# Kernel optimization log

Hardware: AMD Instinct MI355X
Metric: run time of the kernel (lower is better)

The kernel has to match this reference:

```python
import jax, jax.numpy as jnp
import numpy as np

N = 50000      # nodes
E = 800000     # edges (before self loops)
F_IN = 128     # num_features
D = 128        # d_graph_layer
L = 3          # n_graph_layer (extra GAT layers after conv1)
DFC = 128      # d_FC_layer
NFC = 2        # n_FC_layer
C = 2          # num_classes
G = 1000       # number of graphs
NEG_SLOPE = 0.2


def setup_inputs() -> dict:
    key = jax.random.key(0)
    ks = jax.random.split(key, 24)
    s = lambda d: 1.0 / np.sqrt(d)
    inp = {
        "x": jax.random.normal(ks[0], (N, F_IN), jnp.float32),
        "energy": jax.random.normal(ks[1], (G, 1), jnp.float32),
        # conv1 params
        "W1": jax.random.normal(ks[2], (F_IN, D), jnp.float32) * s(F_IN),
        "as1": jax.random.normal(ks[3], (D,), jnp.float32) * s(D),
        "ad1": jax.random.normal(ks[4], (D,), jnp.float32) * s(D),
        "b1": jnp.zeros((D,), jnp.float32),
        # stacked convs params
        "Ws": jax.random.normal(ks[5], (L, D, D), jnp.float32) * s(D),
        "ass": jax.random.normal(ks[6], (L, D), jnp.float32) * s(D),
        "ads": jax.random.normal(ks[7], (L, D), jnp.float32) * s(D),
        "bs": jnp.zeros((L, D), jnp.float32),
        # FC head
        "lin0_W": jax.random.normal(ks[8], (D, DFC), jnp.float32) * s(D),
        "lin0_b": jnp.zeros((DFC,), jnp.float32),
        "lin1_W": jax.random.normal(ks[9], (DFC + 1, DFC), jnp.float32) * s(DFC + 1),
        "lin1_b": jnp.zeros((DFC,), jnp.float32),
        "lins_W": jax.random.normal(ks[10], (NFC - 1, DFC, DFC), jnp.float32) * s(DFC),
        "lins_b": jnp.zeros((NFC - 1, DFC), jnp.float32),
        "lin3_W": jax.random.normal(ks[11], (DFC, C), jnp.float32) * s(DFC),
        "lin3_b": jnp.zeros((C,), jnp.float32),
        # graph structure
        "edge_index": jax.random.randint(ks[12], (2, E), 0, N, dtype=jnp.int64),
        "batchs": jnp.sort(jax.random.randint(ks[13], (N,), 0, G, dtype=jnp.int64)),
    }
    return inp


def gat_layer(x, W, a_src, a_dst, b, src, dst):
    # GATConv (heads=1): h = xW; e_ij = LeakyReLU(a_src.h_src + a_dst.h_dst);
    # alpha = softmax over edges grouped by dst; out_i = sum alpha * h_src + b
    h = x @ W                                        # [N, D]
    e = jax.nn.leaky_relu((h @ a_src)[src] + (h @ a_dst)[dst], NEG_SLOPE)  # [E']
    m = jax.ops.segment_max(e, dst, num_segments=N)  # every node has a self loop
    w = jnp.exp(e - m[dst])
    denom = jax.ops.segment_sum(w, dst, num_segments=N)
    alpha = w / denom[dst]
    out = jax.ops.segment_sum(h[src] * alpha[:, None], dst, num_segments=N)
    return out + b


def reference(x, energy, W1, as1, ad1, b1, Ws, ass, ads, bs,
              lin0_W, lin0_b, lin1_W, lin1_b, lins_W, lins_b,
              lin3_W, lin3_b, edge_index, batchs):
    loop = jnp.arange(N, dtype=edge_index.dtype)     # GATConv add_self_loops
    src = jnp.concatenate([edge_index[0], loop])
    dst = jnp.concatenate([edge_index[1], loop])

    h = jax.nn.relu(gat_layer(x, W1, as1, ad1, b1, src, dst))
    for i in range(L):
        h = jax.nn.relu(gat_layer(h, Ws[i], ass[i], ads[i], bs[i], src, dst))

    g = jax.ops.segment_sum(h, batchs, num_segments=G)   # global_add_pool [G, D]
    y = jax.nn.relu(g @ lin0_W + lin0_b)                 # lins[0]
    z = jax.nn.relu(jnp.concatenate([y, energy], axis=1) @ lin1_W + lin1_b)
    z = z + y                                            # residual
    for i in range(NFC - 1):
        z = jax.nn.relu(z @ lins_W[i] + lins_b[i])
    logits = z @ lin3_W + lin3_b
    return jax.nn.log_softmax(logits, axis=1)            # last == 'log'
```

## Files before the change

kernel.cpp:

```cpp
#include <hip/hip_runtime.h>
#include <math.h>

#define NN 50000
#define EE 800000
#define ET 850000
#define DD 128
#define GG 1000
#define SLOPE 0.2f

typedef unsigned int  u32;
typedef unsigned short u16;

__device__ __forceinline__ u16 f2h(float f){
  return __builtin_bit_cast(unsigned short, (_Float16)f);
}
__device__ __forceinline__ float hlo(u32 d){
  return (float)__builtin_bit_cast(_Float16, (unsigned short)(d & 0xFFFFu));
}
__device__ __forceinline__ float hhi(u32 d){
  return (float)__builtin_bit_cast(_Float16, (unsigned short)(d >> 16));
}

__global__ void init_k(const int* __restrict__ batchs, int* __restrict__ cnt,
                       int* __restrict__ gstart){
  int n = blockIdx.x*256 + threadIdx.x;
  if (n < NN){
    cnt[n] = 0;
    int b = batchs[n];
    int prev = n ? batchs[n-1] : -1;
    for (int g = prev+1; g <= b; ++g) gstart[g] = n;
    if (n == NN-1){
      for (int g = b+1; g <= GG; ++g) gstart[g] = NN;
    }
  }
}

__global__ void count_k(const int* __restrict__ ei, int* __restrict__ cnt){
  int e = blockIdx.x*256 + threadIdx.x;
  if (e < ET){
    int d = (e < EE) ? ei[EE + e] : (e - EE);
    atomicAdd(&cnt[d], 1);
  }
}

__global__ __launch_bounds__(256) void blocksum_k(const int* __restrict__ cnt,
                                                  int* __restrict__ bsum){
  int i = blockIdx.x*256 + threadIdx.x;
  int v = (i < NN) ? cnt[i] : 0;
  #pragma unroll
  for (int o=32;o;o>>=1) v += __shfl_xor(v,o);
  __shared__ int ws[4];
  if ((threadIdx.x & 63) == 0) ws[threadIdx.x>>6] = v;
  __syncthreads();
  if (threadIdx.x == 0) bsum[blockIdx.x] = ws[0]+ws[1]+ws[2]+ws[3];
}

__global__ __launch_bounds__(256) void scanb_k(int* __restrict__ bsum, int nb){
  int tid = threadIdx.x;
  int v = (tid < nb) ? bsum[tid] : 0;
  int lane = tid & 63, wv = tid >> 6;
  int s = v;
  #pragma unroll
  for (int o=1;o<64;o<<=1){ int t = __shfl_up(s,o); if (lane>=o) s += t; }
  __shared__ int ws[4];
  if (lane == 63) ws[wv] = s;
  __syncthreads();
  int woff = 0;
  for (int k=0;k<wv;++k) woff += ws[k];
  if (tid < nb) bsum[tid] = s - v + woff;
}

__global__ __launch_bounds__(256) void scatter_k(const int* __restrict__ cnt,
                                                 const int* __restrict__ bsum,
                                                 int* __restrict__ row_start,
                                                 int* __restrict__ cursor){
  int i = blockIdx.x*256 + threadIdx.x;
  int v = (i < NN) ? cnt[i] : 0;
  int lane = threadIdx.x & 63, wv = threadIdx.x >> 6;
  int s = v;
  #pragma unroll
  for (int o=1;o<64;o<<=1){ int t = __shfl_up(s,o); if (lane>=o) s += t; }
  __shared__ int ws[4];
  if (lane == 63) ws[wv] = s;
  __syncthreads();
  int woff = 0;
  for (int k=0;k<wv;++k) woff += ws[k];
  int off = s - v + woff + bsum[blockIdx.x];
  if (i < NN){ row_start[i] = off; cursor[i] = off; }
  if (i == 0) row_start[NN] = ET;
}

__global__ void fill_k(const int* __restrict__ ei, int* __restrict__ cursor,
                       int* __restrict__ srcs){
  int e = blockIdx.x*256 + threadIdx.x;
  if (e < ET){
    int s, d;
    if (e < EE){ s = ei[e]; d = ei[EE + e]; }
    else       { s = e - EE; d = s; }
    int pos = atomicAdd(&cursor[d], 1);
    srcs[pos] = s;
  }
}

__global__ __launch_bounds__(256) void gemm128_f_k(const float* __restrict__ A,
                                                   const float* __restrict__ W,
                                                   const float* __restrict__ as,
                                                   const float* __restrict__ ad,
                                                   float* __restrict__ C,
                                                   float* __restrict__ hs,
                                                   float* __restrict__ hd){
  __shared__ float Alt[DD*64];
  __shared__ float Wl[DD*64];
  int tid = threadIdx.x;
  int rbase = blockIdx.x*64;
  for (int it=0; it<8; ++it){
    int i = it*256 + tid;
    int r = i & 63;
    int c4 = i >> 6;
    float4 v = {0.f,0.f,0.f,0.f};
    if (rbase + r < NN) v = *(const float4*)(A + (size_t)(rbase+r)*DD + c4*4);
    Alt[(c4*4+0)*64 + r] = v.x;
    Alt[(c4*4+1)*64 + r] = v.y;
    Alt[(c4*4+2)*64 + r] = v.z;
    Alt[(c4*4+3)*64 + r] = v.w;
  }
  int ry = tid >> 4, cx = tid & 15;
  float hsum[4] = {0.f,0.f,0.f,0.f};
  float hdsum[4] = {0.f,0.f,0.f,0.f};
  for (int jt=0; jt<2; ++jt){
    __syncthreads();
    for (int it=0; it<8; ++it){
      int i = it*256 + tid;
      int k = i >> 4, c4 = i & 15;
      *(float4*)(Wl + k*64 + c4*4) = *(const float4*)(W + k*DD + jt*64 + c4*4);
    }
    __syncthreads();
    float acc[4][4] = {};
    #pragma unroll 8
    for (int k=0;k<DD;++k){
      float4 av = *(const float4*)(Alt + k*64 + ry*4);
      float4 wv = *(const float4*)(Wl + k*64 + cx*4);
      float a[4] = {av.x, av.y, av.z, av.w};
      float b[4] = {wv.x, wv.y, wv.z, wv.w};
      #pragma unroll
      for (int ii=0;ii<4;++ii)
        #pragma unroll
        for (int jj=0;jj<4;++jj)
          acc[ii][jj] += a[ii]*b[jj];
    }
    float4 a_s = *(const float4*)(as + jt*64 + cx*4);
    float4 a_d = *(const float4*)(ad + jt*64 + cx*4);
    #pragma unroll
    for (int ii=0;ii<4;++ii){
      float ds = acc[ii][0]*a_s.x + acc[ii][1]*a_s.y + acc[ii][2]*a_s.z + acc[ii][3]*a_s.w;
      float dd = acc[ii][0]*a_d.x + acc[ii][1]*a_d.y + acc[ii][2]*a_d.z + acc[ii][3]*a_d.w;
      #pragma unroll
      for (int o=1;o<16;o<<=1){ ds += __shfl_xor(ds,o); dd += __shfl_xor(dd,o); }
      hsum[ii] += ds; hdsum[ii] += dd;
    }
    #pragma unroll
    for (int ii=0;ii<4;++ii){
      int r = rbase + ry*4 + ii;
      if (r < NN){
        float4 o = {acc[ii][0], acc[ii][1], acc[ii][2], acc[ii][3]};
        *(float4*)(C + (size_t)r*DD + jt*64 + cx*4) = o;
      }
    }
  }
  if (cx == 0){
    #pragma unroll
    for (int ii=0;ii<4;++ii){
      int r = rbase + ry*4 + ii;
      if (r < NN){ hs[r] = hsum[ii]; hd[r] = hdsum[ii]; }
    }
  }
}

__global__ __launch_bounds__(256) void gemm128_h_k(const float* __restrict__ A,
                                                   const float* __restrict__ W,
                                                   const float* __restrict__ as,
                                                   const float* __restrict__ ad,
                                                   u16* __restrict__ Ch,
                                                   float* __restrict__ hs,
                                                   float* __restrict__ hd){
  __shared__ float Alt[DD*64];
  __shared__ float Wl[DD*64];
  int tid = threadIdx.x;
  int rbase = blockIdx.x*64;
  for (int it=0; it<8; ++it){
    int i = it*256 + tid;
    int r = i & 63;
    int c4 = i >> 6;
    float4 v = {0.f,0.f,0.f,0.f};
    if (rbase + r < NN) v = *(const float4*)(A + (size_t)(rbase+r)*DD + c4*4);
    Alt[(c4*4+0)*64 + r] = v.x;
    Alt[(c4*4+1)*64 + r] = v.y;
    Alt[(c4*4+2)*64 + r] = v.z;
    Alt[(c4*4+3)*64 + r] = v.w;
  }
  int ry = tid >> 4, cx = tid & 15;
  float hsum[4] = {0.f,0.f,0.f,0.f};
  float hdsum[4] = {0.f,0.f,0.f,0.f};
  for (int jt=0; jt<2; ++jt){
    __syncthreads();
    for (int it=0; it<8; ++it){
      int i = it*256 + tid;
      int k = i >> 4, c4 = i & 15;
      *(float4*)(Wl + k*64 + c4*4) = *(const float4*)(W + k*DD + jt*64 + c4*4);
    }
    __syncthreads();
    float acc[4][4] = {};
    #pragma unroll 8
    for (int k=0;k<DD;++k){
      float4 av = *(const float4*)(Alt + k*64 + ry*4);
      float4 wv = *(const float4*)(Wl + k*64 + cx*4);
      float a[4] = {av.x, av.y, av.z, av.w};
      float b[4] = {wv.x, wv.y, wv.z, wv.w};
      #pragma unroll
      for (int ii=0;ii<4;++ii)
        #pragma unroll
        for (int jj=0;jj<4;++jj)
          acc[ii][jj] += a[ii]*b[jj];
    }
    float4 a_s = *(const float4*)(as + jt*64 + cx*4);
    float4 a_d = *(const float4*)(ad + jt*64 + cx*4);
    #pragma unroll
    for (int ii=0;ii<4;++ii){
      float ds = acc[ii][0]*a_s.x + acc[ii][1]*a_s.y + acc[ii][2]*a_s.z + acc[ii][3]*a_s.w;
      float dd = acc[ii][0]*a_d.x + acc[ii][1]*a_d.y + acc[ii][2]*a_d.z + acc[ii][3]*a_d.w;
      #pragma unroll
      for (int o=1;o<16;o<<=1){ ds += __shfl_xor(ds,o); dd += __shfl_xor(dd,o); }
      hsum[ii] += ds; hdsum[ii] += dd;
    }
    #pragma unroll
    for (int ii=0;ii<4;++ii){
      int r = rbase + ry*4 + ii;
      if (r < NN){
        ushort4 o;
        o.x = f2h(acc[ii][0]); o.y = f2h(acc[ii][1]);
        o.z = f2h(acc[ii][2]); o.w = f2h(acc[ii][3]);
        *(ushort4*)(Ch + (size_t)r*DD + jt*64 + cx*4) = o;
      }
    }
  }
  if (cx == 0){
    #pragma unroll
    for (int ii=0;ii<4;++ii){
      int r = rbase + ry*4 + ii;
      if (r < NN){ hs[r] = hsum[ii]; hd[r] = hdsum[ii]; }
    }
  }
}

__global__ __launch_bounds__(256) void gat_agg_f_k(const float* __restrict__ h,
                                                   const float* __restrict__ hs,
                                                   const float* __restrict__ hd,
                                                   const int* __restrict__ row_start,
                                                   const int* __restrict__ srcs,
                                                   const float* __restrict__ bias,
                                                   float* __restrict__ out){
  int node = blockIdx.x*4 + (threadIdx.x >> 6);
  int lane = threadIdx.x & 63;
  if (node >= NN) return;
  int half = lane >> 5;
  int hl   = lane & 31;
  int beg = row_start[node], end = row_start[node+1];
  float hdn = hd[node];
  float m = -INFINITY, denom = 0.f;
  float4 acc = {0.f,0.f,0.f,0.f};
  for (int c=beg; c<end; c+=64){
    int nc = min(64, end-c);
    float e = -INFINITY; int src = 0;
    if (lane < nc){
      src = srcs[c+lane];
      float t = hs[src] + hdn;
      e = (t >= 0.f) ? t : SLOPE*t;
    }
    float cm = e;
    #pragma unroll
    for (int o=32;o;o>>=1) cm = fmaxf(cm, __shfl_xor(cm,o));
    float nm = fmaxf(m, cm);
    float w = (lane < nc) ? expf(e - nm) : 0.f;
    float cs = w;
    #pragma unroll
    for (int o=32;o;o>>=1) cs += __shfl_xor(cs,o);
    float scale = expf(m - nm);
    denom = denom*scale + cs;
    acc.x *= scale; acc.y *= scale; acc.z *= scale; acc.w *= scale;
    m = nm;
    int nh = (nc + 1 - half) >> 1;
    for (int i=0;i<nh;++i){
      int j = 2*i + half;
      float wi = __shfl(w, j);
      int   si = __shfl(src, j);
      float4 hv = *(const float4*)(h + (size_t)si*DD + hl*4);
      acc.x += wi*hv.x; acc.y += wi*hv.y; acc.z += wi*hv.z; acc.w += wi*hv.w;
    }
  }
  acc.x += __shfl_xor(acc.x, 32);
  acc.y += __shfl_xor(acc.y, 32);
  acc.z += __shfl_xor(acc.z, 32);
  acc.w += __shfl_xor(acc.w, 32);
  if (half == 0){
    float inv = 1.f/denom;
    float4 b4 = *(const float4*)(bias + hl*4);
    float4 o4;
    o4.x = fmaxf(acc.x*inv + b4.x, 0.f);
    o4.y = fmaxf(acc.y*inv + b4.y, 0.f);
    o4.z = fmaxf(acc.z*inv + b4.z, 0.f);
    o4.w = fmaxf(acc.w*inv + b4.w, 0.f);
    *(float4*)(out + (size_t)node*DD + hl*4) = o4;
  }
}

__global__ __launch_bounds__(256) void gat_agg_h_k(const u16* __restrict__ hh,
                                                   const float* __restrict__ hs,
                                                   const float* __restrict__ hd,
                                                   const int* __restrict__ row_start,
                                                   const int* __restrict__ srcs,
                                                   const float* __restrict__ bias,
                                                   float* __restrict__ out){
  int node = blockIdx.x*4 + (threadIdx.x >> 6);
  int lane = threadIdx.x & 63;
  if (node >= NN) return;
  int half = lane >> 5;
  int hl   = lane & 31;
  int beg = row_start[node], end = row_start[node+1];
  float hdn = hd[node];
  float m = -INFINITY, denom = 0.f;
  float a0=0.f, a1=0.f, a2=0.f, a3=0.f;
  for (int c=beg; c<end; c+=64){
    int nc = min(64, end-c);
    float e = -INFINITY; int src = 0;
    if (lane < nc){
      src = srcs[c+lane];
      float t = hs[src] + hdn;
      e = (t >= 0.f) ? t : SLOPE*t;
    }
    float cm = e;
    #pragma unroll
    for (int o=32;o;o>>=1) cm = fmaxf(cm, __shfl_xor(cm,o));
    float nm = fmaxf(m, cm);
    float w = (lane < nc) ? expf(e - nm) : 0.f;
    float cs = w;
    #pragma unroll
    for (int o=32;o;o>>=1) cs += __shfl_xor(cs,o);
    float scale = expf(m - nm);
    denom = denom*scale + cs;
    a0 *= scale; a1 *= scale; a2 *= scale; a3 *= scale;
    m = nm;
    int nh = (nc + 1 - half) >> 1;
    for (int i=0;i<nh;++i){
      int j = 2*i + half;
      float wi = __shfl(w, j);
      int   si = __shfl(src, j);
      uint2 hv = *(const uint2*)(hh + (size_t)si*DD + hl*4);
      a0 += wi*hlo(hv.x); a1 += wi*hhi(hv.x);
      a2 += wi*hlo(hv.y); a3 += wi*hhi(hv.y);
    }
  }
  a0 += __shfl_xor(a0, 32);
  a1 += __shfl_xor(a1, 32);
  a2 += __shfl_xor(a2, 32);
  a3 += __shfl_xor(a3, 32);
  if (half == 0){
    float inv = 1.f/denom;
    float4 b4 = *(const float4*)(bias + hl*4);
    float4 o4;
    o4.x = fmaxf(a0*inv + b4.x, 0.f);
    o4.y = fmaxf(a1*inv + b4.y, 0.f);
    o4.z = fmaxf(a2*inv + b4.z, 0.f);
    o4.w = fmaxf(a3*inv + b4.w, 0.f);
    *(float4*)(out + (size_t)node*DD + hl*4) = o4;
  }
}

__global__ __launch_bounds__(128) void tail_k(const float* __restrict__ h,
                                              const int* __restrict__ gstart,
                                              const float* __restrict__ energy,
                                              const float* __restrict__ W0, const float* __restrict__ b0,
                                              const float* __restrict__ W1, const float* __restrict__ b1,
                                              const float* __restrict__ W2, const float* __restrict__ b2,
                                              const float* __restrict__ W3, const float* __restrict__ b3,
                                              float* __restrict__ out){
  __shared__ float row[DD];
  __shared__ float buf[DD];
  int gr = blockIdx.x, j = threadIdx.x;
  int beg = gstart[gr], end = gstart[gr+1];
  float s = 0.f;
  for (int n=beg; n<end; ++n) s += h[(size_t)n*DD + j];
  row[j] = s;
  __syncthreads();
  float acc = 0.f;
  #pragma unroll 8
  for (int k=0;k<DD;++k) acc += row[k]*W0[k*DD + j];
  float y = fmaxf(acc + b0[j], 0.f);
  buf[j] = y;
  __syncthreads();
  acc = 0.f;
  #pragma unroll 8
  for (int k=0;k<DD;++k) acc += buf[k]*W1[k*DD + j];
  acc += energy[gr]*W1[DD*DD + j];
  float z = fmaxf(acc + b1[j], 0.f) + y;
  __syncthreads();
  row[j] = z;
  __syncthreads();
  acc = 0.f;
  #pragma unroll 8
  for (int k=0;k<DD;++k) acc += row[k]*W2[k*DD + j];
  float z2 = fmaxf(acc + b2[j], 0.f);
  buf[j] = z2;
  __syncthreads();
  if (j < 64){
    float z0 = buf[j], z1 = buf[j+64];
    float l0 = z0*W3[j*2]     + z1*W3[(j+64)*2];
    float l1 = z0*W3[j*2 + 1] + z1*W3[(j+64)*2 + 1];
    #pragma unroll
    for (int o=32;o;o>>=1){ l0 += __shfl_xor(l0,o); l1 += __shfl_xor(l1,o); }
    if (j == 0){
      l0 += b3[0]; l1 += b3[1];
      float mx = fmaxf(l0, l1);
      float lse = mx + logf(expf(l0-mx) + expf(l1-mx));
      out[gr*2]   = l0 - lse;
      out[gr*2+1] = l1 - lse;
    }
  }
}

extern "C" void kernel_launch(void* const* d_in, const int* in_sizes, int n_in,
                              void* d_out, int out_size, void* d_ws, size_t ws_size,
                              hipStream_t stream) {
  const float* x      = (const float*)d_in[0];
  const float* energy = (const float*)d_in[1];
  const float* W1     = (const float*)d_in[2];
  const float* as1    = (const float*)d_in[3];
  const float* ad1    = (const float*)d_in[4];
  const float* b1     = (const float*)d_in[5];
  const float* Ws     = (const float*)d_in[6];
  const float* ass    = (const float*)d_in[7];
  const float* ads    = (const float*)d_in[8];
  const float* bs     = (const float*)d_in[9];
  const float* lin0_W = (const float*)d_in[10];
  const float* lin0_b = (const float*)d_in[11];
  const float* lin1_W = (const float*)d_in[12];
  const float* lin1_b = (const float*)d_in[13];
  const float* lins_W = (const float*)d_in[14];
  const float* lins_b = (const float*)d_in[15];
  const float* lin3_W = (const float*)d_in[16];
  const float* lin3_b = (const float*)d_in[17];
  const int*   ei     = (const int*)d_in[18];
  const int*   batchs = (const int*)d_in[19];
  float* out = (float*)d_out;

  char* wp = (char*)d_ws;
  auto alloc = [&](size_t bytes)->void*{
    void* p = (void*)wp;
    wp += (bytes + 255) & ~(size_t)255;
    return p;
  };
  float* hA        = (float*)alloc((size_t)NN*DD*4);
  float* hB        = (float*)alloc((size_t)NN*DD*4);
  u16*   hHf       = (u16*)hB;
  float* hs        = (float*)alloc((size_t)NN*4);
  float* hd        = (float*)alloc((size_t)NN*4);
  int*   cnt       = (int*)alloc((size_t)NN*4);
  int*   row_start = (int*)alloc((size_t)(NN+1)*4);
  int*   cursor    = (int*)alloc((size_t)NN*4);
  int*   srcs      = (int*)alloc((size_t)ET*4);
  int*   gstart    = (int*)alloc((size_t)(GG+1)*4);
  int*   bsum      = (int*)alloc((size_t)256*4);

  const int NB_N  = (NN + 255)/256;
  const int NB_E  = (ET + 255)/256;
  const int NB_W  = (NN + 3)/4;
  const int NB_G  = (NN + 63)/64;

  init_k<<<NB_N, 256, 0, stream>>>(batchs, cnt, gstart);
  count_k<<<NB_E, 256, 0, stream>>>(ei, cnt);
  blocksum_k<<<NB_N, 256, 0, stream>>>(cnt, bsum);
  scanb_k<<<1, 256, 0, stream>>>(bsum, NB_N);
  scatter_k<<<NB_N, 256, 0, stream>>>(cnt, bsum, row_start, cursor);
  fill_k<<<NB_E, 256, 0, stream>>>(ei, cursor, srcs);

  gemm128_f_k<<<NB_G, 256, 0, stream>>>(x, W1, as1, ad1, hB, hs, hd);
  gat_agg_f_k<<<NB_W, 256, 0, stream>>>(hB, hs, hd, row_start, srcs, b1, hA);
  gemm128_f_k<<<NB_G, 256, 0, stream>>>(hA, Ws, ass, ads, hB, hs, hd);
  gat_agg_f_k<<<NB_W, 256, 0, stream>>>(hB, hs, hd, row_start, srcs, bs, hA);

  gemm128_h_k<<<NB_G, 256, 0, stream>>>(hA, Ws + (size_t)1*DD*DD, ass + DD, ads + DD,
                                        hHf, hs, hd);
  gat_agg_h_k<<<NB_W, 256, 0, stream>>>(hHf, hs, hd, row_start, srcs, bs + DD, hA);
  gemm128_h_k<<<NB_G, 256, 0, stream>>>(hA, Ws + (size_t)2*DD*DD, ass + 2*DD, ads + 2*DD,
                                        hHf, hs, hd);
  gat_agg_h_k<<<NB_W, 256, 0, stream>>>(hHf, hs, hd, row_start, srcs, bs + 2*DD, hA);

  tail_k<<<GG, 128, 0, stream>>>(hA, gstart, energy,
                                 lin0_W, lin0_b, lin1_W, lin1_b,
                                 lins_W, lins_b, lin3_W, lin3_b, out);
}
```

Before: 587.3 us.

## Build CSR with rank-based positions and two-pass bucketed scatter

The count pass now records each edge's atomic rank, so the final CSR position is row_start plus rank and no second atomic cursor is needed. Edges are then partitioned into 4096-slot position buckets through shared memory (partA) and written out per bucket with coalesced int4 stores (partB). This replaces the random global scattered writes of fill_k with more localized traffic. The cost is an extra rank array, an 8-byte staging buffer and one more kernel launch.

New measurement: 550.6 us. -6.3%, faster.

```diff
diff --git a/kernel.cpp b/kernel.cpp
--- a/kernel.cpp
+++ b/kernel.cpp
@@ -8,6 +8,11 @@
 #define GG 1000
 #define SLOPE 0.2f
 
+#define KB   2048
+#define NBA  416
+#define BSZ  4096
+#define NBUK 208
+
 typedef unsigned int  u32;
 typedef unsigned short u16;
 
@@ -22,8 +27,9 @@
 }
 
 __global__ void init_k(const int* __restrict__ batchs, int* __restrict__ cnt,
-                       int* __restrict__ gstart){
+                       int* __restrict__ gstart, int* __restrict__ bcur){
   int n = blockIdx.x*256 + threadIdx.x;
+  if (n < NBUK) bcur[n] = 0;
   if (n < NN){
     cnt[n] = 0;
     int b = batchs[n];
@@ -35,11 +41,12 @@
   }
 }
 
-__global__ void count_k(const int* __restrict__ ei, int* __restrict__ cnt){
+__global__ void count_k(const int* __restrict__ ei, int* __restrict__ cnt,
+                        int* __restrict__ rank){
   int e = blockIdx.x*256 + threadIdx.x;
   if (e < ET){
     int d = (e < EE) ? ei[EE + e] : (e - EE);
-    atomicAdd(&cnt[d], 1);
+    rank[e] = atomicAdd(&cnt[d], 1);
   }
 }
 
@@ -72,8 +79,7 @@
 
 __global__ __launch_bounds__(256) void scatter_k(const int* __restrict__ cnt,
                                                  const int* __restrict__ bsum,
-                                                 int* __restrict__ row_start,
-                                                 int* __restrict__ cursor){
+                                                 int* __restrict__ row_start){
   int i = blockIdx.x*256 + threadIdx.x;
   int v = (i < NN) ? cnt[i] : 0;
   int lane = threadIdx.x & 63, wv = threadIdx.x >> 6;
@@ -86,19 +92,83 @@
   int woff = 0;
   for (int k=0;k<wv;++k) woff += ws[k];
   int off = s - v + woff + bsum[blockIdx.x];
-  if (i < NN){ row_start[i] = off; cursor[i] = off; }
+  if (i < NN) row_start[i] = off;
   if (i == 0) row_start[NN] = ET;
 }
 
-__global__ void fill_k(const int* __restrict__ ei, int* __restrict__ cursor,
-                       int* __restrict__ srcs){
-  int e = blockIdx.x*256 + threadIdx.x;
-  if (e < ET){
-    int s, d;
-    if (e < EE){ s = ei[e]; d = ei[EE + e]; }
-    else       { s = e - EE; d = s; }
-    int pos = atomicAdd(&cursor[d], 1);
-    srcs[pos] = s;
+__global__ __launch_bounds__(256) void partA_k(const int* __restrict__ ei,
+                                               const int* __restrict__ rank,
+                                               const int* __restrict__ row_start,
+                                               int* __restrict__ bcur,
+                                               uint2* __restrict__ stage){
+  __shared__ uint2 lpairs[KB];
+  __shared__ int lcnt[256], lstart[256], lrun[256], gbase[256];
+  __shared__ int ws[4];
+  int tid = threadIdx.x;
+  int base = blockIdx.x * KB;
+  int nE = min(KB, ET - base);
+  lcnt[tid] = 0;
+  __syncthreads();
+  u32 pos_r[KB/256]; u32 src_r[KB/256];
+  #pragma unroll
+  for (int i=0;i<KB/256;++i){
+    int e = base + i*256 + tid;
+    u32 p = 0xFFFFFFFFu, s = 0;
+    if (e < ET){
+      int d, sr;
+      if (e < EE){ sr = ei[e]; d = ei[EE + e]; }
+      else       { sr = e - EE; d = sr; }
+      p = (u32)(row_start[d] + rank[e]);
+      s = (u32)sr;
+      atomicAdd(&lcnt[p >> 12], 1);
+    }
+    pos_r[i] = p; src_r[i] = s;
+  }
+  __syncthreads();
+  int v = lcnt[tid];
+  int lane = tid & 63, wv = tid >> 6;
+  int s = v;
+  #pragma unroll
+  for (int o=1;o<64;o<<=1){ int t = __shfl_up(s,o); if (lane>=o) s += t; }
+  if (lane == 63) ws[wv] = s;
+  __syncthreads();
+  int woff = 0;
+  for (int k=0;k<wv;++k) woff += ws[k];
+  int excl = s - v + woff;
+  lstart[tid] = excl;
+  lrun[tid]   = excl;
+  gbase[tid]  = (tid < NBUK && v > 0) ? atomicAdd(&bcur[tid], v) : 0;
+  __syncthreads();
+  #pragma unroll
+  for (int i=0;i<KB/256;++i){
+    if (pos_r[i] != 0xFFFFFFFFu){
+      int b = pos_r[i] >> 12;
+      int slot = atomicAdd(&lrun[b], 1);
+      lpairs[slot] = make_uint2(pos_r[i], src_r[i]);
+    }
+  }
+  __syncthreads();
+  for (int j = tid; j < nE; j += 256){
+    uint2 pr = lpairs[j];
+    int b = pr.x >> 12;
+    int dest = (b << 12) + gbase[b] + (j - lstart[b]);
+    stage[dest] = pr;
+  }
+}
+
+__global__ __launch_bounds__(256) void partB_k(const uint2* __restrict__ stage,
+                                               int* __restrict__ srcs){
+  __shared__ int buf[BSZ];
+  int b = blockIdx.x, tid = threadIdx.x;
+  int base = b << 12;
+  int n_b = min(BSZ, ET - base);
+  for (int j = tid; j < n_b; j += 256){
+    uint2 pr = stage[base + j];
+    buf[pr.x - base] = (int)pr.y;
+  }
+  __syncthreads();
+  for (int j = tid; j*4 < n_b; j += 256){
+    *(int4*)(srcs + base + j*4) = *(const int4*)(buf + j*4);
   }
 }
 
@@ -465,8 +535,10 @@
   float* hd        = (float*)alloc((size_t)NN*4);
   int*   cnt       = (int*)alloc((size_t)NN*4);
   int*   row_start = (int*)alloc((size_t)(NN+1)*4);
-  int*   cursor    = (int*)alloc((size_t)NN*4);
+  int*   rank      = (int*)alloc((size_t)ET*4);
   int*   srcs      = (int*)alloc((size_t)ET*4);
+  uint2* stage     = (uint2*)alloc((size_t)NBUK*BSZ*8);
+  int*   bcur      = (int*)alloc((size_t)NBUK*4);
   int*   gstart    = (int*)alloc((size_t)(GG+1)*4);
   int*   bsum      = (int*)alloc((size_t)256*4);
 
@@ -475,12 +547,13 @@
   const int NB_W  = (NN + 3)/4;
   const int NB_G  = (NN + 63)/64;
 
-  init_k<<<NB_N, 256, 0, stream>>>(batchs, cnt, gstart);
-  count_k<<<NB_E, 256, 0, stream>>>(ei, cnt);
+  init_k<<<NB_N, 256, 0, stream>>>(batchs, cnt, gstart, bcur);
+  count_k<<<NB_E, 256, 0, stream>>>(ei, cnt, rank);
   blocksum_k<<<NB_N, 256, 0, stream>>>(cnt, bsum);
   scanb_k<<<1, 256, 0, stream>>>(bsum, NB_N);
-  scatter_k<<<NB_N, 256, 0, stream>>>(cnt, bsum, row_start, cursor);
-  fill_k<<<NB_E, 256, 0, stream>>>(ei, cursor, srcs);
+  scatter_k<<<NB_N, 256, 0, stream>>>(cnt, bsum, row_start);
+  partA_k<<<NBA, 256, 0, stream>>>(ei, rank, row_start, bcur, stage);
+  partB_k<<<NBUK, 256, 0, stream>>>(stage, srcs);
 
   gemm128_f_k<<<NB_G, 256, 0, stream>>>(x, W1, as1, ad1, hB, hs, hd);
   gat_agg_f_k<<<NB_W, 256, 0, stream>>>(hB, hs, hd, row_start, srcs, b1, hA);
```
